# Optimization experiments

Measured on AMD Instinct MI355X. Metric: run time of the kernel, lower is better.

## Reference

```python
import jax, jax.numpy as jnp
import numpy as np

S = 50.0
M = 0.5
EPS = 1e-7
NORM_EPS = 1e-12

B, D = 1024, 512
C, K = 50000, 3


def _l2_normalize(x, axis=-1):
    n = jnp.linalg.norm(x, axis=axis, keepdims=True)
    return x / jnp.maximum(n, NORM_EPS)


def setup_inputs() -> dict:
    key = jax.random.key(0)
    k1, k2, k3 = jax.random.split(key, 3)
    embeddings = jax.random.normal(k1, (B, D), dtype=jnp.float32)
    labels = jax.random.randint(k2, (B,), 0, C, dtype=jnp.int64)
    # xavier_uniform over flattened (C*K, D) view
    limit = float(np.sqrt(6.0 / (C * K + D)))
    weight = jax.random.uniform(k3, (C, K, D), dtype=jnp.float32, minval=-limit, maxval=limit)
    return {"embeddings": embeddings, "labels": labels, "weight": weight}


def reference(embeddings, labels, weight):
    ne = _l2_normalize(embeddings, axis=-1)            # [B, D]
    nw = _l2_normalize(weight, axis=-1)                # [C, K, D] (row-wise over D)
    # cosine similarity expressed as a GEMM, then max over subcenters
    cosine = jnp.einsum('bd,ckd->bck', ne, nw)          # [B, C, K]
    cosine_max = jnp.max(cosine, axis=2)                # [B, C]
    theta = jnp.arccos(jnp.clip(cosine_max, -1.0 + EPS, 1.0 - EPS))
    target_logits = jnp.cos(theta + M)                  # [B, C]
    one_hot = jax.nn.one_hot(labels, C, dtype=cosine_max.dtype)
    return S * (one_hot * target_logits + (1.0 - one_hot) * cosine_max)
```

## Files before the change

### kernel.cpp

```cpp
#include <hip/hip_runtime.h>
#include <stdint.h>

#define B_N   1024
#define D_N   512
#define C_N   50000
#define K_N   3
#define CP    50016
#define NROWS (CP * 4)

#define S_SCALE 50.0f
#define COS_M   0.8775825619f
#define SIN_M   0.4794255386f
#define EPS_C   1e-7f

typedef __bf16 bf16_t;
typedef bf16_t bf16x8 __attribute__((ext_vector_type(8)));
typedef float  f32x4  __attribute__((ext_vector_type(4)));

__device__ __forceinline__ float wave_reduce_sum(float v) {
#pragma unroll
    for (int m = 1; m < 64; m <<= 1) v += __shfl_xor(v, m, 64);
    return v;
}

__device__ __forceinline__ void async_copy16(const void* g, void* l) {
    __builtin_amdgcn_global_load_lds(
        (const __attribute__((address_space(1))) void*)g,
        (__attribute__((address_space(3))) void*)l,
        16, 0, 0);
}

__global__ void k_norm_emb(const float* __restrict__ x, bf16_t* __restrict__ y) {
    const int row  = blockIdx.x * 4 + (threadIdx.x >> 6);
    const int lane = threadIdx.x & 63;
    const float4* p = (const float4*)(x + (size_t)row * D_N + lane * 8);
    float4 a = p[0], b = p[1];
    float s = a.x*a.x + a.y*a.y + a.z*a.z + a.w*a.w
            + b.x*b.x + b.y*b.y + b.z*b.z + b.w*b.w;
    s = wave_reduce_sum(s);
    float sc = 1.0f / fmaxf(sqrtf(s), 1e-12f);
    bf16x8 o;
    o[0] = (bf16_t)(a.x * sc); o[1] = (bf16_t)(a.y * sc);
    o[2] = (bf16_t)(a.z * sc); o[3] = (bf16_t)(a.w * sc);
    o[4] = (bf16_t)(b.x * sc); o[5] = (bf16_t)(b.y * sc);
    o[6] = (bf16_t)(b.z * sc); o[7] = (bf16_t)(b.w * sc);
    *(bf16x8*)(y + (size_t)row * D_N + lane * 8) = o;
}

__global__ void k_norm_w(const float* __restrict__ x, bf16_t* __restrict__ y) {
    const int row  = blockIdx.x * 4 + (threadIdx.x >> 6);
    const int lane = threadIdx.x & 63;
    const float4* p = (const float4*)(x + (size_t)row * D_N + lane * 8);
    float4 a = p[0], b = p[1];
    float s = a.x*a.x + a.y*a.y + a.z*a.z + a.w*a.w
            + b.x*b.x + b.y*b.y + b.z*b.z + b.w*b.w;
    s = wave_reduce_sum(s);
    float sc = 1.0f / fmaxf(sqrtf(s), 1e-12f);
    const size_t orow = (size_t)row + (size_t)(row / 3);
    bf16x8 o;
    o[0] = (bf16_t)(a.x * sc); o[1] = (bf16_t)(a.y * sc);
    o[2] = (bf16_t)(a.z * sc); o[3] = (bf16_t)(a.w * sc);
    o[4] = (bf16_t)(b.x * sc); o[5] = (bf16_t)(b.y * sc);
    o[6] = (bf16_t)(b.z * sc); o[7] = (bf16_t)(b.w * sc);
    *(bf16x8*)(y + orow * D_N + lane * 8) = o;
}

__global__ __launch_bounds__(256) void k_gemm(const bf16_t* __restrict__ Wn,
                                              const bf16_t* __restrict__ En,
                                              const int*    __restrict__ labels,
                                              float*        __restrict__ out) {
    __shared__ bf16_t Ws[128][32];
    __shared__ bf16_t Es[128][32];
    __shared__ float  So[128][33];

    const int tid  = threadIdx.x;
    const int wave = tid >> 6, lane = tid & 63;
    const int wr = wave >> 1, wc = wave & 1;
    const int col  = lane & 15, quad = lane >> 4;

    const int    b0 = blockIdx.x * 128;
    const size_t n0 = (size_t)blockIdx.y * 128;
    const int    c0 = blockIdx.y * 32;

    f32x4 acc[4][4] = {};

    const int srow   = lane >> 2;
    const int schunk = (lane & 3) * 8;

    for (int kk = 0; kk < D_N; kk += 32) {
        __syncthreads();
#pragma unroll
        for (int i = 0; i < 2; ++i) {
            const int rb = i * 64 + wave * 16;
            const bf16_t* ga = Wn + (n0 + rb + srow) * D_N + kk + schunk;
            async_copy16(ga, &Ws[rb][0]);
            const bf16_t* gb = En + (size_t)(b0 + rb + srow) * D_N + kk + schunk;
            async_copy16(gb, &Es[rb][0]);
        }
        __syncthreads();

        bf16x8 af[4], bfr[4];
#pragma unroll
        for (int t = 0; t < 4; ++t) {
            af[t]  = *(const bf16x8*)&Ws[wr * 64 + t * 16 + col][quad * 8];
            bfr[t] = *(const bf16x8*)&Es[wc * 64 + t * 16 + col][quad * 8];
        }
#pragma unroll
        for (int ti = 0; ti < 4; ++ti)
#pragma unroll
            for (int tj = 0; tj < 4; ++tj)
                acc[ti][tj] = __builtin_amdgcn_mfma_f32_16x16x32_bf16(
                    af[ti], bfr[tj], acc[ti][tj], 0, 0, 0);
    }

    int lab[4];
#pragma unroll
    for (int tj = 0; tj < 4; ++tj) lab[tj] = labels[b0 + wc * 64 + tj * 16 + col];

#pragma unroll
    for (int ti = 0; ti < 4; ++ti) {
        const int c_local = wr * 16 + ti * 4 + quad;
        const int c       = c0 + c_local;
#pragma unroll
        for (int tj = 0; tj < 4; ++tj) {
            float v = fmaxf(fmaxf(acc[ti][tj][0], acc[ti][tj][1]), acc[ti][tj][2]);
            if (c == lab[tj]) {
                float x = fminf(fmaxf(v, -1.0f + EPS_C), 1.0f - EPS_C);
                v = x * COS_M - sqrtf(fmaxf(1.0f - x * x, 0.0f)) * SIN_M;
            }
            So[wc * 64 + tj * 16 + col][c_local] = S_SCALE * v;
        }
    }
    __syncthreads();

    const int row  = tid >> 1;
    const int half = tid & 1;
    const size_t gbase = (size_t)(b0 + row) * C_N;
#pragma unroll
    for (int q = 0; q < 4; ++q) {
        const int ci = half * 16 + q * 4;
        const int c  = c0 + ci;
        if (c < C_N) {
            float4 o = make_float4(So[row][ci], So[row][ci + 1],
                                   So[row][ci + 2], So[row][ci + 3]);
            *(float4*)(out + gbase + c) = o;
        }
    }
}

__global__ void k_fb_norms(const float* __restrict__ emb, const float* __restrict__ w,
                           float* __restrict__ einv, float* __restrict__ winv) {
    const int row  = blockIdx.x * 4 + (threadIdx.x >> 6);
    const int lane = threadIdx.x & 63;
    if (row >= B_N + C_N * K_N) return;
    const float* src = (row < B_N) ? (emb + (size_t)row * D_N)
                                   : (w + (size_t)(row - B_N) * D_N);
    const float4* p = (const float4*)(src + lane * 8);
    float4 a = p[0], b = p[1];
    float s = a.x*a.x + a.y*a.y + a.z*a.z + a.w*a.w
            + b.x*b.x + b.y*b.y + b.z*b.z + b.w*b.w;
    s = wave_reduce_sum(s);
    if (lane == 0) {
        float sc = 1.0f / fmaxf(sqrtf(s), 1e-12f);
        if (row < B_N) einv[row] = sc; else winv[row - B_N] = sc;
    }
}

__global__ void k_fb_gemm(const float* __restrict__ emb, const float* __restrict__ w,
                          const int* __restrict__ labels, const float* __restrict__ einv,
                          const float* __restrict__ winv, float* __restrict__ out) {
    const int b = blockIdx.x;
    const int c = blockIdx.y * 256 + threadIdx.x;
    if (c >= C_N) return;
    const float4* e4 = (const float4*)(emb + (size_t)b * D_N);
    const float es = einv[b];
    float best = -1e30f;
    for (int k = 0; k < K_N; ++k) {
        const float4* w4 = (const float4*)(w + ((size_t)c * K_N + k) * D_N);
        float dot = 0.0f;
#pragma unroll 4
        for (int d = 0; d < D_N / 4; ++d) {
            float4 a = e4[d], bb = w4[d];
            dot += a.x*bb.x + a.y*bb.y + a.z*bb.z + a.w*bb.w;
        }
        dot *= es * winv[c * K_N + k];
        best = fmaxf(best, dot);
    }
    if (c == labels[b]) {
        float x = fminf(fmaxf(best, -1.0f + EPS_C), 1.0f - EPS_C);
        best = x * COS_M - sqrtf(fmaxf(1.0f - x * x, 0.0f)) * SIN_M;
    }
    out[(size_t)b * C_N + c] = S_SCALE * best;
}

extern "C" void kernel_launch(void* const* d_in, const int* in_sizes, int n_in,
                              void* d_out, int out_size, void* d_ws, size_t ws_size,
                              hipStream_t stream) {
    const float* emb    = (const float*)d_in[0];
    const int*   labels = (const int*)d_in[1];
    const float* weight = (const float*)d_in[2];
    float*       out    = (float*)d_out;

    const size_t offW = (size_t)1 << 20;
    const size_t need = offW + (size_t)NROWS * D_N * 2;
    if (ws_size >= need) {
        bf16_t* En = (bf16_t*)d_ws;
        bf16_t* Wn = (bf16_t*)((char*)d_ws + offW);
        k_norm_emb<<<B_N / 4, 256, 0, stream>>>(emb, En);
        k_norm_w<<<(C_N * K_N) / 4, 256, 0, stream>>>(weight, Wn);
        k_gemm<<<dim3(B_N / 128, NROWS / 128), 256, 0, stream>>>(Wn, En, labels, out);
    } else {
        float* einv = (float*)d_ws;
        float* winv = einv + B_N;
        k_fb_norms<<<(B_N + C_N * K_N) / 4, 256, 0, stream>>>(emb, weight, einv, winv);
        k_fb_gemm<<<dim3(B_N, (C_N + 255) / 256), 256, 0, stream>>>(emb, weight, labels,
                                                                    einv, winv, out);
    }
}
```

Baseline: 774.8 us.

## Drop subcenter padding, enlarge weight tiles, swizzle grid, fuse norm kernels

Removes the 4th padded subcenter row per class, so the GEMM covers 192 weight rows (64 classes) per block instead of 128 padded rows, cutting wasted MFMA work and weight bytes by a quarter. The two normalization kernels become one launch. Blocks are remapped with a swizzle so the 8 batch tiles sharing a weight slab run close together for L2 reuse. The epilogue does the max over subcenters through per-wave shared scratch and writes output with nontemporal stores, and the input loads are also nontemporal. The cost is more accumulator registers (6x4 tiles) and a more complex epilogue. The unpadded weight rows sit past 150000, so the last slab reads uninitialized workspace, but those columns are masked out.

```diff
diff --git a/kernel.cpp b/kernel.cpp
--- a/kernel.cpp
+++ b/kernel.cpp
@@ -5,8 +5,10 @@
 #define D_N   512
 #define C_N   50000
 #define K_N   3
-#define CP    50016
-#define NROWS (CP * 4)
+
+#define SLABS 784
+#define NR    (SLABS * 192)
+#define GRID_G (SLABS * 8)
 
 #define S_SCALE 50.0f
 #define COS_M   0.8775825619f
@@ -30,120 +32,124 @@
         16, 0, 0);
 }
 
-__global__ void k_norm_emb(const float* __restrict__ x, bf16_t* __restrict__ y) {
+__global__ void k_norm(const float* __restrict__ emb, const float* __restrict__ w,
+                       bf16_t* __restrict__ En, bf16_t* __restrict__ Wn) {
     const int row  = blockIdx.x * 4 + (threadIdx.x >> 6);
     const int lane = threadIdx.x & 63;
-    const float4* p = (const float4*)(x + (size_t)row * D_N + lane * 8);
-    float4 a = p[0], b = p[1];
-    float s = a.x*a.x + a.y*a.y + a.z*a.z + a.w*a.w
-            + b.x*b.x + b.y*b.y + b.z*b.z + b.w*b.w;
+    const float* src;
+    bf16_t*      dst;
+    if (row < B_N) {
+        src = emb + (size_t)row * D_N;
+        dst = En  + (size_t)row * D_N;
+    } else {
+        const int r = row - B_N;
+        src = w  + (size_t)r * D_N;
+        dst = Wn + (size_t)r * D_N;
+    }
+    const f32x4* p = (const f32x4*)(src + lane * 8);
+    f32x4 a = __builtin_nontemporal_load(p);
+    f32x4 b = __builtin_nontemporal_load(p + 1);
+    float s = a[0]*a[0] + a[1]*a[1] + a[2]*a[2] + a[3]*a[3]
+            + b[0]*b[0] + b[1]*b[1] + b[2]*b[2] + b[3]*b[3];
     s = wave_reduce_sum(s);
-    float sc = 1.0f / fmaxf(sqrtf(s), 1e-12f);
+    const float sc = 1.0f / fmaxf(sqrtf(s), 1e-12f);
     bf16x8 o;
-    o[0] = (bf16_t)(a.x * sc); o[1] = (bf16_t)(a.y * sc);
-    o[2] = (bf16_t)(a.z * sc); o[3] = (bf16_t)(a.w * sc);
-    o[4] = (bf16_t)(b.x * sc); o[5] = (bf16_t)(b.y * sc);
-    o[6] = (bf16_t)(b.z * sc); o[7] = (bf16_t)(b.w * sc);
-    *(bf16x8*)(y + (size_t)row * D_N + lane * 8) = o;
-}
-
-__global__ void k_norm_w(const float* __restrict__ x, bf16_t* __restrict__ y) {
-    const int row  = blockIdx.x * 4 + (threadIdx.x >> 6);
-    const int lane = threadIdx.x & 63;
-    const float4* p = (const float4*)(x + (size_t)row * D_N + lane * 8);
-    float4 a = p[0], b = p[1];
-    float s = a.x*a.x + a.y*a.y + a.z*a.z + a.w*a.w
-            + b.x*b.x + b.y*b.y + b.z*b.z + b.w*b.w;
-    s = wave_reduce_sum(s);
-    float sc = 1.0f / fmaxf(sqrtf(s), 1e-12f);
-    const size_t orow = (size_t)row + (size_t)(row / 3);
-    bf16x8 o;
-    o[0] = (bf16_t)(a.x * sc); o[1] = (bf16_t)(a.y * sc);
-    o[2] = (bf16_t)(a.z * sc); o[3] = (bf16_t)(a.w * sc);
-    o[4] = (bf16_t)(b.x * sc); o[5] = (bf16_t)(b.y * sc);
-    o[6] = (bf16_t)(b.z * sc); o[7] = (bf16_t)(b.w * sc);
-    *(bf16x8*)(y + orow * D_N + lane * 8) = o;
+    o[0] = (bf16_t)(a[0]*sc); o[1] = (bf16_t)(a[1]*sc);
+    o[2] = (bf16_t)(a[2]*sc); o[3] = (bf16_t)(a[3]*sc);
+    o[4] = (bf16_t)(b[0]*sc); o[5] = (bf16_t)(b[1]*sc);
+    o[6] = (bf16_t)(b[2]*sc); o[7] = (bf16_t)(b[3]*sc);
+    *(bf16x8*)(dst + lane * 8) = o;
 }
 
 __global__ __launch_bounds__(256) void k_gemm(const bf16_t* __restrict__ Wn,
                                               const bf16_t* __restrict__ En,
                                               const int*    __restrict__ labels,
                                               float*        __restrict__ out) {
-    __shared__ bf16_t Ws[128][32];
-    __shared__ bf16_t Es[128][32];
-    __shared__ float  So[128][33];
+    __shared__ union {
+        struct { bf16_t W[192][32]; bf16_t E[128][32]; } st;
+        float sw[4][16][100];
+    } sh;
 
     const int tid  = threadIdx.x;
     const int wave = tid >> 6, lane = tid & 63;
     const int wr = wave >> 1, wc = wave & 1;
-    const int col  = lane & 15, quad = lane >> 4;
-
-    const int    b0 = blockIdx.x * 128;
-    const size_t n0 = (size_t)blockIdx.y * 128;
-    const int    c0 = blockIdx.y * 32;
-
-    f32x4 acc[4][4] = {};
-
-    const int srow   = lane >> 2;
-    const int schunk = (lane & 3) * 8;
+    const int col = lane & 15, quad = lane >> 4;
+
+    const int l  = blockIdx.x;
+    const int r8 = l & 7, g = l >> 3;
+    const int s  = (g >> 3) * 8 + r8;
+    const int bt = g & 7;
+    const size_t n0 = (size_t)s * 192;
+    const int c0 = s * 64;
+    const int b0 = bt * 128;
+
+    f32x4 acc[6][4] = {};
+
+    const int srow = lane >> 2, schunk = (lane & 3) * 8;
 
     for (int kk = 0; kk < D_N; kk += 32) {
         __syncthreads();
 #pragma unroll
+        for (int i = 0; i < 3; ++i) {
+            const int rb = (wave * 3 + i) * 16;
+            async_copy16(Wn + (n0 + rb + srow) * D_N + kk + schunk, &sh.st.W[rb][0]);
+        }
+#pragma unroll
         for (int i = 0; i < 2; ++i) {
-            const int rb = i * 64 + wave * 16;
-            const bf16_t* ga = Wn + (n0 + rb + srow) * D_N + kk + schunk;
-            async_copy16(ga, &Ws[rb][0]);
-            const bf16_t* gb = En + (size_t)(b0 + rb + srow) * D_N + kk + schunk;
-            async_copy16(gb, &Es[rb][0]);
+            const int rb = (wave * 2 + i) * 16;
+            async_copy16(En + (size_t)(b0 + rb + srow) * D_N + kk + schunk, &sh.st.E[rb][0]);
         }
         __syncthreads();
 
-        bf16x8 af[4], bfr[4];
-#pragma unroll
-        for (int t = 0; t < 4; ++t) {
-            af[t]  = *(const bf16x8*)&Ws[wr * 64 + t * 16 + col][quad * 8];
-            bfr[t] = *(const bf16x8*)&Es[wc * 64 + t * 16 + col][quad * 8];
-        }
-#pragma unroll
-        for (int ti = 0; ti < 4; ++ti)
+        bf16x8 af[6], bfr[4];
+#pragma unroll
+        for (int ti = 0; ti < 6; ++ti)
+            af[ti] = *(const bf16x8*)&sh.st.W[wr * 96 + ti * 16 + col][quad * 8];
+#pragma unroll
+        for (int tj = 0; tj < 4; ++tj)
+            bfr[tj] = *(const bf16x8*)&sh.st.E[wc * 64 + tj * 16 + col][quad * 8];
+
+#pragma unroll
+        for (int ti = 0; ti < 6; ++ti)
 #pragma unroll
             for (int tj = 0; tj < 4; ++tj)
                 acc[ti][tj] = __builtin_amdgcn_mfma_f32_16x16x32_bf16(
                     af[ti], bfr[tj], acc[ti][tj], 0, 0, 0);
     }
 
-    int lab[4];
-#pragma unroll
-    for (int tj = 0; tj < 4; ++tj) lab[tj] = labels[b0 + wc * 64 + tj * 16 + col];
-
-#pragma unroll
-    for (int ti = 0; ti < 4; ++ti) {
-        const int c_local = wr * 16 + ti * 4 + quad;
-        const int c       = c0 + c_local;
-#pragma unroll
-        for (int tj = 0; tj < 4; ++tj) {
-            float v = fmaxf(fmaxf(acc[ti][tj][0], acc[ti][tj][1]), acc[ti][tj][2]);
-            if (c == lab[tj]) {
-                float x = fminf(fmaxf(v, -1.0f + EPS_C), 1.0f - EPS_C);
-                v = x * COS_M - sqrtf(fmaxf(1.0f - x * x, 0.0f)) * SIN_M;
+    __syncthreads();
+
+    float* sw = &sh.sw[wave][0][0];
+    const int bb = lane >> 2, p = lane & 3;
+
+#pragma unroll
+    for (int tj = 0; tj < 4; ++tj) {
+        asm volatile("s_waitcnt lgkmcnt(0)" ::: "memory");
+#pragma unroll
+        for (int ti = 0; ti < 6; ++ti)
+            *(f32x4*)&sw[col * 100 + ti * 16 + quad * 4] = acc[ti][tj];
+        asm volatile("s_waitcnt lgkmcnt(0)" ::: "memory");
+
+        const int b   = b0 + wc * 64 + tj * 16 + bb;
+        const int lab = labels[b];
+        const float* rowp = &sw[bb * 100 + 24 * p];
+#pragma unroll
+        for (int j = 0; j < 2; ++j) {
+            f32x4 o;
+#pragma unroll
+            for (int e = 0; e < 4; ++e) {
+                const int off = 12 * j + 3 * e;
+                float v = fmaxf(fmaxf(rowp[off], rowp[off + 1]), rowp[off + 2]);
+                const int cg = c0 + wr * 32 + 8 * p + 4 * j + e;
+                if (cg == lab) {
+                    float x = fminf(fmaxf(v, -1.0f + EPS_C), 1.0f - EPS_C);
+                    v = x * COS_M - sqrtf(fmaxf(1.0f - x * x, 0.0f)) * SIN_M;
+                }
+                o[e] = S_SCALE * v;
             }
-            So[wc * 64 + tj * 16 + col][c_local] = S_SCALE * v;
-        }
-    }
-    __syncthreads();
-
-    const int row  = tid >> 1;
-    const int half = tid & 1;
-    const size_t gbase = (size_t)(b0 + row) * C_N;
-#pragma unroll
-    for (int q = 0; q < 4; ++q) {
-        const int ci = half * 16 + q * 4;
-        const int c  = c0 + ci;
-        if (c < C_N) {
-            float4 o = make_float4(So[row][ci], So[row][ci + 1],
-                                   So[row][ci + 2], So[row][ci + 3]);
-            *(float4*)(out + gbase + c) = o;
+            const int cbase = c0 + wr * 32 + 8 * p + 4 * j;
+            if (cbase + 3 < C_N)
+                __builtin_nontemporal_store(o, (f32x4*)(out + (size_t)b * C_N + cbase));
         }
     }
 }
@@ -202,17 +208,16 @@
     float*       out    = (float*)d_out;
 
     const size_t offW = (size_t)1 << 20;
-    const size_t need = offW + (size_t)NROWS * D_N * 2;
+    const size_t need = offW + (size_t)NR * D_N * 2;
     if (ws_size >= need) {
         bf16_t* En = (bf16_t*)d_ws;
         bf16_t* Wn = (bf16_t*)((char*)d_ws + offW);
-        k_norm_emb<<<B_N / 4, 256, 0, stream>>>(emb, En);
-        k_norm_w<<<(C_N * K_N) / 4, 256, 0, stream>>>(weight, Wn);
-        k_gemm<<<dim3(B_N / 128, NROWS / 128), 256, 0, stream>>>(Wn, En, labels, out);
+        k_norm<<<(B_N + C_N * K_N) / 4, 256, 0, stream>>>(emb, weight, En, Wn);
+        k_gemm<<<GRID_G, 256, 0, stream>>>(Wn, En, labels, out);
     } else {
         float* einv = (float*)d_ws;
         float* winv = einv + B_N;
-        k_fb_norms<<<(B_N + C_N * K_N) / 4, 256, 0, stream>>>(emb, weight, einv, winv);
+        k_fb_norms<<<(B_N + C_N * K_N + 3) / 4, 256, 0, stream>>>(emb, weight, einv, winv);
         k_fb_gemm<<<dim3(B_N, (C_N + 255) / 256), 256, 0, stream>>>(emb, weight, labels,
                                                                     einv, winv, out);
     }
```

Measured after the change: 1.117 ms. +44.2%, slower.
